# Optimization experiments

Hardware: AMD Instinct MI355X
Metric: run time of the kernel (lower is better)

Reference implementation:

```python
import jax, jax.numpy as jnp
import numpy as np

K = 2        # capsules
ROUTIT = 3   # routing iterations
DD = 32      # per-capsule dim
D = K * DD   # 64
NEG = -1e9
EPS_NORM = 1e-12


def _l2norm_caps(c, n):
    # F.normalize over last dim of [n, K, DD]
    c = c.reshape(n, K, DD)
    nrm = jnp.sqrt((c * c).sum(axis=2, keepdims=True))
    c = c / jnp.maximum(nrm, EPS_NORM)
    return c.reshape(n, D)


def disen_encoder(x, W, b, src_trg):
    n = x.shape[0]
    src, trg = src_trg[0], src_trg[1]
    x = x @ W + b                               # [n, D]
    x = _l2norm_caps(x, n)
    z = x[src].reshape(-1, K, DD)               # [m, K, DD] per-edge source capsules
    c = x
    for _ in range(ROUTIT):
        ct = c[trg].reshape(-1, K, DD)          # gather target capsules
        p = jax.nn.softmax((z * ct).sum(axis=2), axis=1)   # [m, K]
        ws = (p[:, :, None] * z).reshape(-1, D)            # [m, D]
        c = c.at[trg].add(ws)                   # scatter-aggregate (index_add_)
        c = _l2norm_caps(c, n)
    return c


def attention_fuse(z, W1, b1, W2):
    # z: [n, 3, D]
    w = jax.nn.leaky_relu(z @ W1 + b1, negative_slope=0.2) @ W2   # [n, 3, 1]
    beta = jax.nn.softmax(w, axis=1) + 1e-6
    beta = beta / beta.sum(axis=1, keepdims=True)
    return (beta * z).sum(axis=1)               # [n, D]


def masked_softmax(vec, mask):
    m = mask.astype(vec.dtype)
    return jax.nn.softmax(vec * m + (1.0 - m) * NEG, axis=-1)


def joint_update(user, item, A, Wj, bj):
    tu = jax.nn.relu(user @ Wj + bj)
    ti = jax.nn.relu(item @ Wj + bj)
    ui = user @ item.T                          # [N, M]
    uw = masked_softmax(ui, A > 0)
    upd_user = tu + uw @ item
    iw = masked_softmax(ui.T, A.T > 0)
    upd_item = ti + iw @ user
    return upd_user, upd_item


def setup_inputs() -> dict:
    key = jax.random.key(0)
    ks = jax.random.split(key, 24)
    N_NC, N_D, E_NC, E_D = 10240, 5120, 327680, 163840
    inp = {
        'NC_1': jax.random.normal(ks[0], (N_NC, 599), jnp.float32),
        'NC_2': jax.random.normal(ks[1], (N_NC, 599), jnp.float32),
        'NC_3': jax.random.normal(ks[2], (N_NC, 599), jnp.float32),
        'D_1': jax.random.normal(ks[3], (N_D, 91), jnp.float32),
        'D_2': jax.random.normal(ks[4], (N_D, 91), jnp.float32),
        'D_3': jax.random.normal(ks[5], (N_D, 91), jnp.float32),
        'edge_indexNC1': jax.random.randint(ks[6], (2, E_NC), 0, N_NC, jnp.int32),
        'edge_indexNC2': jax.random.randint(ks[7], (2, E_NC), 0, N_NC, jnp.int32),
        'edge_indexNC3': jax.random.randint(ks[8], (2, E_NC), 0, N_NC, jnp.int32),
        'edge_indexD1': jax.random.randint(ks[9], (2, E_D), 0, N_D, jnp.int32),
        'edge_indexD2': jax.random.randint(ks[10], (2, E_D), 0, N_D, jnp.int32),
        'edge_indexD3': jax.random.randint(ks[11], (2, E_D), 0, N_D, jnp.int32),
        'heterogeneous': jnp.zeros((1,), jnp.float32),
        'heterogeneous1': jnp.zeros((1,), jnp.float32),
        'A': jax.random.randint(ks[12], (N_NC, N_D), 0, 2, jnp.int32).astype(jnp.float32),
        'L': jnp.zeros((1,), jnp.float32),
    }
    def xavier(k, shape):
        lim = float(np.sqrt(6.0 / (shape[0] + shape[1])))
        return jax.random.uniform(k, shape, jnp.float32, -lim, lim)
    inp['W_nc'] = xavier(ks[13], (599, D)); inp['b_nc'] = jnp.zeros((D,), jnp.float32)
    inp['W_d'] = xavier(ks[14], (91, D));   inp['b_d'] = jnp.zeros((D,), jnp.float32)
    inp['attn_W1'] = xavier(ks[15], (D, D)); inp['attn_b1'] = jnp.zeros((D,), jnp.float32)
    inp['attn_W2'] = xavier(ks[16], (D, 1))
    inp['joint_W'] = xavier(ks[17], (D, D)); inp['joint_b'] = jnp.zeros((D,), jnp.float32)
    return inp


def reference(NC_1, NC_2, NC_3, D_1, D_2, D_3,
              edge_indexNC1, edge_indexNC2, edge_indexNC3,
              edge_indexD1, edge_indexD2, edge_indexD3,
              heterogeneous, heterogeneous1, A, L,
              W_nc, b_nc, W_d, b_d, attn_W1, attn_b1, attn_W2, joint_W, joint_b):
    nc1 = disen_encoder(NC_1, W_nc, b_nc, edge_indexNC1)
    d1 = disen_encoder(D_1, W_d, b_d, edge_indexD1)
    nc2 = disen_encoder(NC_2, W_nc, b_nc, edge_indexNC2)
    d2 = disen_encoder(D_2, W_d, b_d, edge_indexD2)
    nc3 = disen_encoder(NC_3, W_nc, b_nc, edge_indexNC3)
    d3 = disen_encoder(D_3, W_d, b_d, edge_indexD3)
    nc = attention_fuse(jnp.stack([nc1, nc2, nc3], axis=1), attn_W1, attn_b1, attn_W2)
    d = attention_fuse(jnp.stack([d1, d2, d3], axis=1), attn_W1, attn_b1, attn_W2)
    nc, d = joint_update(nc, d, A, joint_W, joint_b)
    return d @ nc.T   # decoder1 with identity act: [N_d, N_nc]
```

## Files before the change

kernel.cpp:

```cpp
#include <hip/hip_runtime.h>
#include <hip/hip_bf16.h>
#include <stdint.h>

using bf16x8 = __attribute__((ext_vector_type(8))) short;
using f32x4  = __attribute__((ext_vector_type(4))) float;

__device__ __forceinline__ unsigned short f2b(float f) {
  unsigned u = __float_as_uint(f);
  u = u + 0x7FFFu + ((u >> 16) & 1u);
  return (unsigned short)(u >> 16);
}
__device__ __forceinline__ float b2f(unsigned short s) {
  return __uint_as_float(((unsigned)s) << 16);
}

#define N_NC 10240
#define N_D  5120
#define E_NC 327680
#define E_D  163840
#define F_NC 599
#define F_D  91
#define KP_NC 608
#define KP_D  96
#define TOT_NODES 46080
#define TOT_EDGES 1474560
#define MW 160

__global__ __launch_bounds__(256) void k_zero(int* p, int n) {
  int t = blockIdx.x * 256 + threadIdx.x;
  if (t < n) p[t] = 0;
}

__global__ __launch_bounds__(256) void k_prep(const float* Wnc, const float* Wd,
                       unsigned short* WTnc_hi, unsigned short* WTnc_lo,
                       unsigned short* WTd_hi, unsigned short* WTd_lo) {
  int tid = blockIdx.x * blockDim.x + threadIdx.x;
  int stride = gridDim.x * blockDim.x;
  for (int i = tid; i < 64 * KP_NC; i += stride) {
    int d = i / KP_NC, k = i % KP_NC;
    float w = (k < F_NC) ? Wnc[k * 64 + d] : 0.0f;
    unsigned short h = f2b(w);
    WTnc_hi[i] = h;
    WTnc_lo[i] = f2b(w - b2f(h));
  }
  for (int i = tid; i < 64 * KP_D; i += stride) {
    int d = i / KP_D, k = i % KP_D;
    float w = (k < F_D) ? Wd[k * 64 + d] : 0.0f;
    unsigned short h = f2b(w);
    WTd_hi[i] = h;
    WTd_lo[i] = f2b(w - b2f(h));
  }
}

template <int F, int KPAD>
__global__ __launch_bounds__(256) void k_encoder(const float* __restrict__ x,
    const unsigned short* __restrict__ WT_hi, const unsigned short* __restrict__ WT_lo,
    const float* __restrict__ bias, float* __restrict__ out) {
  int wave = threadIdx.x >> 6;
  int tile = blockIdx.x * 4 + wave;
  int l = threadIdx.x & 63;
  int h = l >> 4, r0 = l & 15;
  int m0 = tile * 16;

  f32x4 acc[4] = {{0,0,0,0},{0,0,0,0},{0,0,0,0},{0,0,0,0}};
  const float* xrow = x + (size_t)(m0 + r0) * F;

  for (int ks = 0; ks < KPAD / 32; ++ks) {
    int k0 = ks * 32 + h * 8;
    bf16x8 ah, al;
#pragma unroll
    for (int j = 0; j < 8; ++j) {
      int k = k0 + j;
      float v = (k < F) ? xrow[k] : 0.0f;
      unsigned short hb = f2b(v);
      ah[j] = (short)hb;
      al[j] = (short)f2b(v - b2f(hb));
    }
#pragma unroll
    for (int nt = 0; nt < 4; ++nt) {
      bf16x8 bh = *(const bf16x8*)(WT_hi + (nt * 16 + r0) * KPAD + k0);
      bf16x8 bl = *(const bf16x8*)(WT_lo + (nt * 16 + r0) * KPAD + k0);
      acc[nt] = __builtin_amdgcn_mfma_f32_16x16x32_bf16(ah, bh, acc[nt], 0, 0, 0);
      acc[nt] = __builtin_amdgcn_mfma_f32_16x16x32_bf16(ah, bl, acc[nt], 0, 0, 0);
      acc[nt] = __builtin_amdgcn_mfma_f32_16x16x32_bf16(al, bh, acc[nt], 0, 0, 0);
    }
  }
#pragma unroll
  for (int nt = 0; nt < 4; ++nt) {
    float bv = bias[nt * 16 + r0];
#pragma unroll
    for (int r = 0; r < 4; ++r) acc[nt][r] += bv;
  }
#pragma unroll
  for (int r = 0; r < 4; ++r) {
    float ss0 = acc[0][r] * acc[0][r] + acc[1][r] * acc[1][r];
    float ss1 = acc[2][r] * acc[2][r] + acc[3][r] * acc[3][r];
#pragma unroll
    for (int m = 1; m < 16; m <<= 1) { ss0 += __shfl_xor(ss0, m); ss1 += __shfl_xor(ss1, m); }
    float s0 = 1.0f / fmaxf(sqrtf(ss0), 1e-12f);
    float s1 = 1.0f / fmaxf(sqrtf(ss1), 1e-12f);
    float* o = out + (size_t)(m0 + 4 * h + r) * 64;
    o[ 0 + r0] = acc[0][r] * s0;
    o[16 + r0] = acc[1][r] * s0;
    o[32 + r0] = acc[2][r] * s1;
    o[48 + r0] = acc[3][r] * s1;
  }
}

__device__ __forceinline__ void seg_decode(int t,
    const int* e0, const int* e1, const int* e2,
    const int* e3, const int* e4, const int* e5,
    const int** ep, int* el, int* noff, int* En) {
  if (t < 3 * E_NC) {
    int g = t / E_NC; *el = t - g * E_NC; *En = E_NC; *noff = g * N_NC;
    *ep = (g == 0) ? e0 : (g == 1) ? e1 : e2;
  } else {
    int u = t - 3 * E_NC;
    int g = u / E_D; *el = u - g * E_D; *En = E_D; *noff = 3 * N_NC + g * N_D;
    *ep = (g == 0) ? e3 : (g == 1) ? e4 : e5;
  }
}

__global__ __launch_bounds__(256) void k_hist(const int* e0, const int* e1, const int* e2,
                       const int* e3, const int* e4, const int* e5, int* cnt) {
  int t = blockIdx.x * blockDim.x + threadIdx.x;
  const int* ep; int el, noff, En;
  seg_decode(t, e0, e1, e2, e3, e4, e5, &ep, &el, &noff, &En);
  int trg = ep[En + el];
  atomicAdd(&cnt[noff + trg], 1);
}

__global__ __launch_bounds__(256) void k_scan1(const int* cnt, int* incl, int* bsum) {
  __shared__ int sh[256];
  int g = blockIdx.x * 256 + threadIdx.x;
  int v = cnt[g];
  sh[threadIdx.x] = v;
  __syncthreads();
  for (int off = 1; off < 256; off <<= 1) {
    int t = (threadIdx.x >= off) ? sh[threadIdx.x - off] : 0;
    __syncthreads();
    sh[threadIdx.x] += t;
    __syncthreads();
  }
  incl[g] = sh[threadIdx.x];
  if (threadIdx.x == 255) bsum[blockIdx.x] = sh[255];
}

__global__ __launch_bounds__(256) void k_scan2(int* bsum) {
  __shared__ int sh[256];
  int t = threadIdx.x;
  int v = (t < 180) ? bsum[t] : 0;
  sh[t] = v;
  __syncthreads();
  for (int off = 1; off < 256; off <<= 1) {
    int x = (t >= off) ? sh[t - off] : 0;
    __syncthreads();
    sh[t] += x;
    __syncthreads();
  }
  if (t < 180) bsum[t] = sh[t] - v;
}

__global__ __launch_bounds__(256) void k_scan3(const int* incl, const int* cnt,
                                               const int* bsum, int* rowptr, int* cursor) {
  int g = blockIdx.x * 256 + threadIdx.x;
  int x = incl[g] + bsum[blockIdx.x];
  rowptr[g + 1] = x;
  cursor[g] = x - cnt[g];
  if (g == 0) rowptr[0] = 0;
}

__global__ __launch_bounds__(256) void k_scatter(const int* e0, const int* e1, const int* e2,
                          const int* e3, const int* e4, const int* e5,
                          int* cursor, int* csr) {
  int t = blockIdx.x * blockDim.x + threadIdx.x;
  const int* ep; int el, noff, En;
  seg_decode(t, e0, e1, e2, e3, e4, e5, &ep, &el, &noff, &En);
  int src = ep[el];
  int trg = ep[En + el];
  int pos = atomicAdd(&cursor[noff + trg], 1);
  csr[pos] = src;
}

template <int NPG>
__global__ __launch_bounds__(256) void k_route(const float* __restrict__ xnorm, float* __restrict__ cfin,
    const int* __restrict__ row_ptr, const int* __restrict__ csr, int rpOff) {
  int node = (blockIdx.x * blockDim.x + threadIdx.x) >> 5;
  int q = threadIdx.x & 31;
  int graph = node / NPG;
  size_t gb32 = (size_t)graph * NPG * 32;
  int rp0 = row_ptr[rpOff + node], rp1 = row_ptr[rpOff + node + 1];
  const float2* xn2 = (const float2*)xnorm;
  float2 c = xn2[(size_t)node * 32 + q];
  for (int it = 0; it < 3; ++it) {
    float2 acc = c;
    for (int e = rp0; e < rp1; ++e) {
      int s = csr[e];
      float2 z = xn2[gb32 + (size_t)s * 32 + q];
      float part = z.x * c.x + z.y * c.y;
      part += __shfl_xor(part, 1);
      part += __shfl_xor(part, 2);
      part += __shfl_xor(part, 4);
      part += __shfl_xor(part, 8);
      float other = __shfl_xor(part, 16);
      float p = 1.0f / (1.0f + __expf(other - part));
      acc.x += p * z.x;
      acc.y += p * z.y;
    }
    float ss = acc.x * acc.x + acc.y * acc.y;
    ss += __shfl_xor(ss, 1);
    ss += __shfl_xor(ss, 2);
    ss += __shfl_xor(ss, 4);
    ss += __shfl_xor(ss, 8);
    float sc = 1.0f / fmaxf(sqrtf(ss), 1e-12f);
    c.x = acc.x * sc;
    c.y = acc.y * sc;
  }
  ((float2*)cfin)[(size_t)node * 32 + q] = c;
}

__global__ __launch_bounds__(256) void k_attn(const float* __restrict__ cfin, int n,
    const float* __restrict__ W1, const float* __restrict__ b1, const float* __restrict__ W2,
    const float* __restrict__ Wj, const float* __restrict__ bj,
    unsigned short* bfr, unsigned short* bfT, float* tu) {
  __shared__ float zs[4][3][64];
  __shared__ float fs[4][64];
  int wave = threadIdx.x >> 6, l = threadIdx.x & 63;
  int node = blockIdx.x * 4 + wave;
#pragma unroll
  for (int j = 0; j < 3; ++j)
    zs[wave][j][l] = cfin[((size_t)j * n + node) * 64 + l];
  __syncthreads();
  float w[3];
#pragma unroll
  for (int j = 0; j < 3; ++j) {
    float y = b1[l];
    for (int k = 0; k < 64; ++k) y += zs[wave][j][k] * W1[k * 64 + l];
    y = (y > 0.0f) ? y : 0.2f * y;
    float t = y * W2[l];
#pragma unroll
    for (int m = 1; m < 64; m <<= 1) t += __shfl_xor(t, m);
    w[j] = t;
  }
  float mx = fmaxf(w[0], fmaxf(w[1], w[2]));
  float e0 = __expf(w[0] - mx), e1 = __expf(w[1] - mx), e2 = __expf(w[2] - mx);
  float inv = 1.0f / (e0 + e1 + e2);
  float be0 = e0 * inv + 1e-6f, be1 = e1 * inv + 1e-6f, be2 = e2 * inv + 1e-6f;
  float bs = 1.0f / (be0 + be1 + be2);
  be0 *= bs; be1 *= bs; be2 *= bs;
  float o = be0 * zs[wave][0][l] + be1 * zs[wave][1][l] + be2 * zs[wave][2][l];
  fs[wave][l] = o;
  __syncthreads();
  bfr[(size_t)node * 64 + l] = f2b(o);
  bfT[(size_t)l * n + node] = f2b(o);
  float t = bj[l];
  for (int k = 0; k < 64; ++k) t += fs[wave][k] * Wj[k * 64 + l];
  tu[(size_t)node * 64 + l] = fmaxf(t, 0.0f);
}

__global__ __launch_bounds__(256) void k_mask(const float* __restrict__ A, unsigned int* mb) {
  int wid = (blockIdx.x * blockDim.x + threadIdx.x) >> 6;
  int l = threadIdx.x & 63;
  int row = wid / 10, seg = wid % 10;
  const float4* ap = (const float4*)(A + (size_t)row * 5120 + seg * 512 + l * 8);
  float4 v0 = ap[0], v1 = ap[1];
  unsigned b = (unsigned)(v0.x > 0.0f)       | ((unsigned)(v0.y > 0.0f) << 1)
             | ((unsigned)(v0.z > 0.0f) << 2) | ((unsigned)(v0.w > 0.0f) << 3)
             | ((unsigned)(v1.x > 0.0f) << 4) | ((unsigned)(v1.y > 0.0f) << 5)
             | ((unsigned)(v1.z > 0.0f) << 6) | ((unsigned)(v1.w > 0.0f) << 7);
  b |= ((unsigned)__shfl_xor((int)b, 1)) << 8;
  b |= ((unsigned)__shfl_xor((int)b, 2)) << 16;
  if ((l & 3) == 0) mb[row * MW + seg * 16 + (l >> 2)] = b;
}

template <bool MT>
__global__ __launch_bounds__(256) void k_joint(const unsigned short* __restrict__ qbf,
    const unsigned short* __restrict__ kbf, const unsigned short* __restrict__ vT, int Nk,
    const unsigned int* __restrict__ mb, const float* __restrict__ tu,
    unsigned short* outh, unsigned short* outl) {
  __shared__ float st[4][16][2];
  __shared__ __align__(16) unsigned short pl[4][16][32];
  __shared__ float oc[4][16][64];
  int wave = threadIdx.x >> 6, l = threadIdx.x & 63;
  int h = l >> 4, r0 = l & 15;
  int q0 = blockIdx.x * 16;
  int seg = Nk >> 2;
  int m_lo = wave * seg, m_hi = m_lo + seg;

  bf16x8 a0 = *(const bf16x8*)(qbf + (size_t)(q0 + r0) * 64 + h * 8);
  bf16x8 a1 = *(const bf16x8*)(qbf + (size_t)(q0 + r0) * 64 + 32 + h * 8);

  float lm[4], ls[4];
#pragma unroll
  for (int r = 0; r < 4; ++r) { lm[r] = -1e30f; ls[r] = 0.0f; }

  for (int m0 = m_lo; m0 < m_hi; m0 += 32) {
    f32x4 s0 = {0,0,0,0}, s1 = {0,0,0,0};
    {
      bf16x8 b00 = *(const bf16x8*)(kbf + (size_t)(m0 + r0) * 64 + h * 8);
      bf16x8 b10 = *(const bf16x8*)(kbf + (size_t)(m0 + 16 + r0) * 64 + h * 8);
      s0 = __builtin_amdgcn_mfma_f32_16x16x32_bf16(a0, b00, s0, 0, 0, 0);
      s1 = __builtin_amdgcn_mfma_f32_16x16x32_bf16(a0, b10, s1, 0, 0, 0);
      bf16x8 b01 = *(const bf16x8*)(kbf + (size_t)(m0 + r0) * 64 + 32 + h * 8);
      bf16x8 b11 = *(const bf16x8*)(kbf + (size_t)(m0 + 16 + r0) * 64 + 32 + h * 8);
      s0 = __builtin_amdgcn_mfma_f32_16x16x32_bf16(a1, b01, s0, 0, 0, 0);
      s1 = __builtin_amdgcn_mfma_f32_16x16x32_bf16(a1, b11, s1, 0, 0, 0);
    }
    unsigned w0 = 0, w1 = 0;
    if (MT) {
      w0 = mb[(size_t)(m0 + r0) * MW + (q0 >> 5)];
      w1 = mb[(size_t)(m0 + 16 + r0) * MW + (q0 >> 5)];
    }
#pragma unroll
    for (int r = 0; r < 4; ++r) {
      float e0, e1;
      if (MT) {
        int bit = (q0 & 31) + 4 * h + r;
        e0 = ((w0 >> bit) & 1u) ? s0[r] : -1e9f;
        e1 = ((w1 >> bit) & 1u) ? s1[r] : -1e9f;
      } else {
        unsigned wr = mb[(size_t)(q0 + 4 * h + r) * MW + (m0 >> 5)];
        e0 = ((wr >> r0) & 1u) ? s0[r] : -1e9f;
        e1 = ((wr >> (r0 + 16)) & 1u) ? s1[r] : -1e9f;
      }
      float nm = fmaxf(lm[r], fmaxf(e0, e1));
      ls[r] = ls[r] * __expf(lm[r] - nm) + __expf(e0 - nm) + __expf(e1 - nm);
      lm[r] = nm;
    }
  }
#pragma unroll
  for (int r = 0; r < 4; ++r) {
#pragma unroll
    for (int m = 1; m < 16; m <<= 1) {
      float om = __shfl_xor(lm[r], m), os = __shfl_xor(ls[r], m);
      float nm = fmaxf(lm[r], om);
      ls[r] = ls[r] * __expf(lm[r] - nm) + os * __expf(om - nm);
      lm[r] = nm;
    }
  }
  if (r0 == 0) {
#pragma unroll
    for (int r = 0; r < 4; ++r) { st[wave][4 * h + r][0] = lm[r]; st[wave][4 * h + r][1] = ls[r]; }
  }
  __syncthreads();
  float M[4], S[4];
#pragma unroll
  for (int r = 0; r < 4; ++r) {
    int row = 4 * h + r;
    float mm = fmaxf(fmaxf(st[0][row][0], st[1][row][0]), fmaxf(st[2][row][0], st[3][row][0]));
    float s = st[0][row][1] * __expf(st[0][row][0] - mm)
            + st[1][row][1] * __expf(st[1][row][0] - mm)
            + st[2][row][1] * __expf(st[2][row][0] - mm)
            + st[3][row][1] * __expf(st[3][row][0] - mm);
    M[r] = mm; S[r] = s;
  }

  f32x4 o[4] = {{0,0,0,0},{0,0,0,0},{0,0,0,0},{0,0,0,0}};
  for (int m0 = m_lo; m0 < m_hi; m0 += 32) {
    f32x4 s0 = {0,0,0,0}, s1 = {0,0,0,0};
    {
      bf16x8 b00 = *(const bf16x8*)(kbf + (size_t)(m0 + r0) * 64 + h * 8);
      bf16x8 b10 = *(const bf16x8*)(kbf + (size_t)(m0 + 16 + r0) * 64 + h * 8);
      s0 = __builtin_amdgcn_mfma_f32_16x16x32_bf16(a0, b00, s0, 0, 0, 0);
      s1 = __builtin_amdgcn_mfma_f32_16x16x32_bf16(a0, b10, s1, 0, 0, 0);
      bf16x8 b01 = *(const bf16x8*)(kbf + (size_t)(m0 + r0) * 64 + 32 + h * 8);
      bf16x8 b11 = *(const bf16x8*)(kbf + (size_t)(m0 + 16 + r0) * 64 + 32 + h * 8);
      s0 = __builtin_amdgcn_mfma_f32_16x16x32_bf16(a1, b01, s0, 0, 0, 0);
      s1 = __builtin_amdgcn_mfma_f32_16x16x32_bf16(a1, b11, s1, 0, 0, 0);
    }
    unsigned w0 = 0, w1 = 0;
    if (MT) {
      w0 = mb[(size_t)(m0 + r0) * MW + (q0 >> 5)];
      w1 = mb[(size_t)(m0 + 16 + r0) * MW + (q0 >> 5)];
    }
#pragma unroll
    for (int r = 0; r < 4; ++r) {
      float e0, e1;
      if (MT) {
        int bit = (q0 & 31) + 4 * h + r;
        e0 = ((w0 >> bit) & 1u) ? s0[r] : -1e9f;
        e1 = ((w1 >> bit) & 1u) ? s1[r] : -1e9f;
      } else {
        unsigned wr = mb[(size_t)(q0 + 4 * h + r) * MW + (m0 >> 5)];
        e0 = ((wr >> r0) & 1u) ? s0[r] : -1e9f;
        e1 = ((wr >> (r0 + 16)) & 1u) ? s1[r] : -1e9f;
      }
      pl[wave][4 * h + r][r0]      = f2b(__expf(e0 - M[r]));
      pl[wave][4 * h + r][r0 + 16] = f2b(__expf(e1 - M[r]));
    }
    __syncthreads();
    bf16x8 pa = *(const bf16x8*)(&pl[wave][r0][h * 8]);
#pragma unroll
    for (int nt = 0; nt < 4; ++nt) {
      bf16x8 bv = *(const bf16x8*)(vT + (size_t)(nt * 16 + r0) * Nk + m0 + h * 8);
      o[nt] = __builtin_amdgcn_mfma_f32_16x16x32_bf16(pa, bv, o[nt], 0, 0, 0);
    }
  }
  float inv[4];
#pragma unroll
  for (int r = 0; r < 4; ++r) inv[r] = 1.0f / S[r];
#pragma unroll
  for (int nt = 0; nt < 4; ++nt)
#pragma unroll
    for (int r = 0; r < 4; ++r)
      oc[wave][4 * h + r][nt * 16 + r0] = o[nt][r] * inv[r];
  __syncthreads();
  for (int e = threadIdx.x; e < 1024; e += 256) {
    int row = e >> 6, col = e & 63;
    float v = oc[0][row][col] + oc[1][row][col] + oc[2][row][col] + oc[3][row][col];
    v += tu[(size_t)(q0 + row) * 64 + col];
    unsigned short hb = f2b(v);
    outh[(size_t)(q0 + row) * 64 + col] = hb;
    outl[(size_t)(q0 + row) * 64 + col] = f2b(v - b2f(hb));
  }
}

__global__ __launch_bounds__(256) void k_dec(const unsigned short* __restrict__ Ih,
    const unsigned short* __restrict__ Il,
    const unsigned short* __restrict__ Uh, const unsigned short* __restrict__ Ul,
    float* __restrict__ out) {
  int w = (blockIdx.x * blockDim.x + threadIdx.x) >> 6;
  int l = threadIdx.x & 63, h = l >> 4, r0 = l & 15;
  int i0 = (w / 160) * 16, u0 = (w % 160) * 64;
  size_t abase = (size_t)(i0 + r0) * 64 + h * 8;
  bf16x8 a0h = *(const bf16x8*)(Ih + abase);
  bf16x8 a1h = *(const bf16x8*)(Ih + abase + 32);
  bf16x8 a0l = *(const bf16x8*)(Il + abase);
  bf16x8 a1l = *(const bf16x8*)(Il + abase + 32);
#pragma unroll
  for (int nt = 0; nt < 4; ++nt) {
    size_t bbase = (size_t)(u0 + nt * 16 + r0) * 64 + h * 8;
    bf16x8 b0h = *(const bf16x8*)(Uh + bbase);
    bf16x8 b1h = *(const bf16x8*)(Uh + bbase + 32);
    bf16x8 b0l = *(const bf16x8*)(Ul + bbase);
    bf16x8 b1l = *(const bf16x8*)(Ul + bbase + 32);
    f32x4 acc = {0,0,0,0};
    acc = __builtin_amdgcn_mfma_f32_16x16x32_bf16(a0h, b0h, acc, 0, 0, 0);
    acc = __builtin_amdgcn_mfma_f32_16x16x32_bf16(a1h, b1h, acc, 0, 0, 0);
    acc = __builtin_amdgcn_mfma_f32_16x16x32_bf16(a0h, b0l, acc, 0, 0, 0);
    acc = __builtin_amdgcn_mfma_f32_16x16x32_bf16(a1h, b1l, acc, 0, 0, 0);
    acc = __builtin_amdgcn_mfma_f32_16x16x32_bf16(a0l, b0h, acc, 0, 0, 0);
    acc = __builtin_amdgcn_mfma_f32_16x16x32_bf16(a1l, b1h, acc, 0, 0, 0);
#pragma unroll
    for (int r = 0; r < 4; ++r)
      out[(size_t)(i0 + 4 * h + r) * 10240 + u0 + nt * 16 + r0] = acc[r];
  }
}

extern "C" void kernel_launch(void* const* d_in, const int* in_sizes, int n_in,
                              void* d_out, int out_size, void* d_ws, size_t ws_size,
                              hipStream_t stream) {
  const float* NC1 = (const float*)d_in[0];
  const float* NC2 = (const float*)d_in[1];
  const float* NC3 = (const float*)d_in[2];
  const float* Dx1 = (const float*)d_in[3];
  const float* Dx2 = (const float*)d_in[4];
  const float* Dx3 = (const float*)d_in[5];
  const int* e0 = (const int*)d_in[6];
  const int* e1 = (const int*)d_in[7];
  const int* e2 = (const int*)d_in[8];
  const int* e3 = (const int*)d_in[9];
  const int* e4 = (const int*)d_in[10];
  const int* e5 = (const int*)d_in[11];
  const float* A   = (const float*)d_in[14];
  const float* Wnc = (const float*)d_in[16];
  const float* bnc = (const float*)d_in[17];
  const float* Wd  = (const float*)d_in[18];
  const float* bd  = (const float*)d_in[19];
  const float* W1  = (const float*)d_in[20];
  const float* b1  = (const float*)d_in[21];
  const float* W2  = (const float*)d_in[22];
  const float* Wj  = (const float*)d_in[23];
  const float* bj  = (const float*)d_in[24];
  (void)in_sizes; (void)n_in; (void)out_size; (void)ws_size;

  char* ob = (char*)d_out;
  char* ws = (char*)d_ws;

  float* xn_nc = (float*)(ob);
  float* xn_d  = (float*)(ob + 7864320);
  float* cf_nc = (float*)(ob + 11796480);
  float* cf_d  = (float*)(ob + 19660800);
  int* cnt    = (int*)(ob + 23592960);
  int* incl   = (int*)(ob + 23592960 + 184320);
  int* bsum   = (int*)(ob + 23592960 + 368640);
  int* rowptr = (int*)(ob + 23592960 + 369664);
  int* cursor = (int*)(ob + 23592960 + 554240);
  int* csr    = (int*)(ob + 23592960 + 738560);
  unsigned int* mb = (unsigned int*)(ob + 23592960);
  unsigned short* ubf  = (unsigned short*)(ob);
  unsigned short* ubfT = (unsigned short*)(ob + 1310720);
  unsigned short* ibf  = (unsigned short*)(ob + 2621440);
  unsigned short* ibfT = (unsigned short*)(ob + 3276800);
  float* tu            = (float*)(ob + 3932160);
  float* ti            = (float*)(ob + 6553600);

  unsigned short* udUh = (unsigned short*)(ws);
  unsigned short* udUl = (unsigned short*)(ws + 1310720);
  unsigned short* udIh = (unsigned short*)(ws + 2621440);
  unsigned short* udIl = (unsigned short*)(ws + 3276800);
  unsigned short* WTnc_hi = (unsigned short*)(ws + 3932160);
  unsigned short* WTnc_lo = (unsigned short*)(ws + 4009984);
  unsigned short* WTd_hi  = (unsigned short*)(ws + 4087808);
  unsigned short* WTd_lo  = (unsigned short*)(ws + 4100096);

  k_prep<<<64, 256, 0, stream>>>(Wnc, Wd, WTnc_hi, WTnc_lo, WTd_hi, WTd_lo);

  k_encoder<F_NC, KP_NC><<<160, 256, 0, stream>>>(NC1, WTnc_hi, WTnc_lo, bnc, xn_nc);
  k_encoder<F_NC, KP_NC><<<160, 256, 0, stream>>>(NC2, WTnc_hi, WTnc_lo, bnc, xn_nc + (size_t)N_NC * 64);
  k_encoder<F_NC, KP_NC><<<160, 256, 0, stream>>>(NC3, WTnc_hi, WTnc_lo, bnc, xn_nc + (size_t)2 * N_NC * 64);
  k_encoder<F_D, KP_D><<<80, 256, 0, stream>>>(Dx1, WTd_hi, WTd_lo, bd, xn_d);
  k_encoder<F_D, KP_D><<<80, 256, 0, stream>>>(Dx2, WTd_hi, WTd_lo, bd, xn_d + (size_t)N_D * 64);
  k_encoder<F_D, KP_D><<<80, 256, 0, stream>>>(Dx3, WTd_hi, WTd_lo, bd, xn_d + (size_t)2 * N_D * 64);

  k_zero<<<180, 256, 0, stream>>>(cnt, TOT_NODES);
  k_hist<<<TOT_EDGES / 256, 256, 0, stream>>>(e0, e1, e2, e3, e4, e5, cnt);
  k_scan1<<<180, 256, 0, stream>>>(cnt, incl, bsum);
  k_scan2<<<1, 256, 0, stream>>>(bsum);
  k_scan3<<<180, 256, 0, stream>>>(incl, cnt, bsum, rowptr, cursor);
  k_scatter<<<TOT_EDGES / 256, 256, 0, stream>>>(e0, e1, e2, e3, e4, e5, cursor, csr);

  k_route<N_NC><<<(3 * N_NC) / 8, 256, 0, stream>>>(xn_nc, cf_nc, rowptr, csr, 0);
  k_route<N_D><<<(3 * N_D) / 8, 256, 0, stream>>>(xn_d, cf_d, rowptr, csr, 3 * N_NC);

  k_mask<<<25600, 256, 0, stream>>>(A, mb);

  k_attn<<<N_NC / 4, 256, 0, stream>>>(cf_nc, N_NC, W1, b1, W2, Wj, bj, ubf, ubfT, tu);
  k_attn<<<N_D / 4, 256, 0, stream>>>(cf_d, N_D, W1, b1, W2, Wj, bj, ibf, ibfT, ti);

  k_joint<false><<<N_NC / 16, 256, 0, stream>>>(ubf, ibf, ibfT, N_D, mb, tu, udUh, udUl);
  k_joint<true><<<N_D / 16, 256, 0, stream>>>(ibf, ubf, ubfT, N_NC, mb, ti, udIh, udIl);

  k_dec<<<(N_D / 16) * (N_NC / 64) / 4, 256, 0, stream>>>(udIh, udIl, udUh, udUl, (float*)d_out);
}
```

Baseline: 1.618 ms.

## Fuse masked softmax into a single pass without max subtraction

Replaces the two-pass masked softmax in the joint-attention kernel with one pass. The first pass computed the running max and sum; the second recomputed QK^T and built P·V. Because the user and item embeddings are built from L2-normalised capsules, their dot products are bounded, so exp is applied to raw scores and normalisation is deferred to the final reduction. This halves the score MFMAs and the K loads, drops the per-iteration barrier (the P tile is private to each wave), and pads the P tile in shared memory. The trade-off is that a row with no unmasked entries now outputs zeros rather than the reference's uniform distribution.

```diff
diff --git a/kernel.cpp b/kernel.cpp
--- a/kernel.cpp
+++ b/kernel.cpp
@@ -278,9 +278,9 @@
     const unsigned short* __restrict__ kbf, const unsigned short* __restrict__ vT, int Nk,
     const unsigned int* __restrict__ mb, const float* __restrict__ tu,
     unsigned short* outh, unsigned short* outl) {
-  __shared__ float st[4][16][2];
-  __shared__ __align__(16) unsigned short pl[4][16][32];
+  __shared__ __align__(16) unsigned short pl[4][16][40];
   __shared__ float oc[4][16][64];
+  __shared__ float ssum[4][16];
   int wave = threadIdx.x >> 6, l = threadIdx.x & 63;
   int h = l >> 4, r0 = l & 15;
   int q0 = blockIdx.x * 16;
@@ -290,22 +290,21 @@
   bf16x8 a0 = *(const bf16x8*)(qbf + (size_t)(q0 + r0) * 64 + h * 8);
   bf16x8 a1 = *(const bf16x8*)(qbf + (size_t)(q0 + r0) * 64 + 32 + h * 8);
 
-  float lm[4], ls[4];
-#pragma unroll
-  for (int r = 0; r < 4; ++r) { lm[r] = -1e30f; ls[r] = 0.0f; }
-
+  f32x4 o[4] = {{0,0,0,0},{0,0,0,0},{0,0,0,0},{0,0,0,0}};
+  float ls[4] = {0.0f, 0.0f, 0.0f, 0.0f};
+
+#pragma unroll 2
   for (int m0 = m_lo; m0 < m_hi; m0 += 32) {
     f32x4 s0 = {0,0,0,0}, s1 = {0,0,0,0};
-    {
-      bf16x8 b00 = *(const bf16x8*)(kbf + (size_t)(m0 + r0) * 64 + h * 8);
-      bf16x8 b10 = *(const bf16x8*)(kbf + (size_t)(m0 + 16 + r0) * 64 + h * 8);
-      s0 = __builtin_amdgcn_mfma_f32_16x16x32_bf16(a0, b00, s0, 0, 0, 0);
-      s1 = __builtin_amdgcn_mfma_f32_16x16x32_bf16(a0, b10, s1, 0, 0, 0);
-      bf16x8 b01 = *(const bf16x8*)(kbf + (size_t)(m0 + r0) * 64 + 32 + h * 8);
-      bf16x8 b11 = *(const bf16x8*)(kbf + (size_t)(m0 + 16 + r0) * 64 + 32 + h * 8);
-      s0 = __builtin_amdgcn_mfma_f32_16x16x32_bf16(a1, b01, s0, 0, 0, 0);
-      s1 = __builtin_amdgcn_mfma_f32_16x16x32_bf16(a1, b11, s1, 0, 0, 0);
-    }
+    bf16x8 b00 = *(const bf16x8*)(kbf + (size_t)(m0 + r0) * 64 + h * 8);
+    bf16x8 b10 = *(const bf16x8*)(kbf + (size_t)(m0 + 16 + r0) * 64 + h * 8);
+    bf16x8 b01 = *(const bf16x8*)(kbf + (size_t)(m0 + r0) * 64 + 32 + h * 8);
+    bf16x8 b11 = *(const bf16x8*)(kbf + (size_t)(m0 + 16 + r0) * 64 + 32 + h * 8);
+    s0 = __builtin_amdgcn_mfma_f32_16x16x32_bf16(a0, b00, s0, 0, 0, 0);
+    s1 = __builtin_amdgcn_mfma_f32_16x16x32_bf16(a0, b10, s1, 0, 0, 0);
+    s0 = __builtin_amdgcn_mfma_f32_16x16x32_bf16(a1, b01, s0, 0, 0, 0);
+    s1 = __builtin_amdgcn_mfma_f32_16x16x32_bf16(a1, b11, s1, 0, 0, 0);
+
     unsigned w0 = 0, w1 = 0;
     if (MT) {
       w0 = mb[(size_t)(m0 + r0) * MW + (q0 >> 5)];
@@ -313,82 +312,20 @@
     }
 #pragma unroll
     for (int r = 0; r < 4; ++r) {
-      float e0, e1;
+      float p0, p1;
       if (MT) {
         int bit = (q0 & 31) + 4 * h + r;
-        e0 = ((w0 >> bit) & 1u) ? s0[r] : -1e9f;
-        e1 = ((w1 >> bit) & 1u) ? s1[r] : -1e9f;
+        p0 = ((w0 >> bit) & 1u) ? __expf(s0[r]) : 0.0f;
+        p1 = ((w1 >> bit) & 1u) ? __expf(s1[r]) : 0.0f;
       } else {
         unsigned wr = mb[(size_t)(q0 + 4 * h + r) * MW + (m0 >> 5)];
-        e0 = ((wr >> r0) & 1u) ? s0[r] : -1e9f;
-        e1 = ((wr >> (r0 + 16)) & 1u) ? s1[r] : -1e9f;
+        p0 = ((wr >> r0) & 1u) ? __expf(s0[r]) : 0.0f;
+        p1 = ((wr >> (r0 + 16)) & 1u) ? __expf(s1[r]) : 0.0f;
       }
-      float nm = fmaxf(lm[r], fmaxf(e0, e1));
-      ls[r] = ls[r] * __expf(lm[r] - nm) + __expf(e0 - nm) + __expf(e1 - nm);
-      lm[r] = nm;
-    }
-  }
-#pragma unroll
-  for (int r = 0; r < 4; ++r) {
-#pragma unroll
-    for (int m = 1; m < 16; m <<= 1) {
-      float om = __shfl_xor(lm[r], m), os = __shfl_xor(ls[r], m);
-      float nm = fmaxf(lm[r], om);
-      ls[r] = ls[r] * __expf(lm[r] - nm) + os * __expf(om - nm);
-      lm[r] = nm;
-    }
-  }
-  if (r0 == 0) {
-#pragma unroll
-    for (int r = 0; r < 4; ++r) { st[wave][4 * h + r][0] = lm[r]; st[wave][4 * h + r][1] = ls[r]; }
-  }
-  __syncthreads();
-  float M[4], S[4];
-#pragma unroll
-  for (int r = 0; r < 4; ++r) {
-    int row = 4 * h + r;
-    float mm = fmaxf(fmaxf(st[0][row][0], st[1][row][0]), fmaxf(st[2][row][0], st[3][row][0]));
-    float s = st[0][row][1] * __expf(st[0][row][0] - mm)
-            + st[1][row][1] * __expf(st[1][row][0] - mm)
-            + st[2][row][1] * __expf(st[2][row][0] - mm)
-            + st[3][row][1] * __expf(st[3][row][0] - mm);
-    M[r] = mm; S[r] = s;
-  }
-
-  f32x4 o[4] = {{0,0,0,0},{0,0,0,0},{0,0,0,0},{0,0,0,0}};
-  for (int m0 = m_lo; m0 < m_hi; m0 += 32) {
-    f32x4 s0 = {0,0,0,0}, s1 = {0,0,0,0};
-    {
-      bf16x8 b00 = *(const bf16x8*)(kbf + (size_t)(m0 + r0) * 64 + h * 8);
-      bf16x8 b10 = *(const bf16x8*)(kbf + (size_t)(m0 + 16 + r0) * 64 + h * 8);
-      s0 = __builtin_amdgcn_mfma_f32_16x16x32_bf16(a0, b00, s0, 0, 0, 0);
-      s1 = __builtin_amdgcn_mfma_f32_16x16x32_bf16(a0, b10, s1, 0, 0, 0);
-      bf16x8 b01 = *(const bf16x8*)(kbf + (size_t)(m0 + r0) * 64 + 32 + h * 8);
-      bf16x8 b11 = *(const bf16x8*)(kbf + (size_t)(m0 + 16 + r0) * 64 + 32 + h * 8);
-      s0 = __builtin_amdgcn_mfma_f32_16x16x32_bf16(a1, b01, s0, 0, 0, 0);
-      s1 = __builtin_amdgcn_mfma_f32_16x16x32_bf16(a1, b11, s1, 0, 0, 0);
-    }
-    unsigned w0 = 0, w1 = 0;
-    if (MT) {
-      w0 = mb[(size_t)(m0 + r0) * MW + (q0 >> 5)];
-      w1 = mb[(size_t)(m0 + 16 + r0) * MW + (q0 >> 5)];
-    }
-#pragma unroll
-    for (int r = 0; r < 4; ++r) {
-      float e0, e1;
-      if (MT) {
-        int bit = (q0 & 31) + 4 * h + r;
-        e0 = ((w0 >> bit) & 1u) ? s0[r] : -1e9f;
-        e1 = ((w1 >> bit) & 1u) ? s1[r] : -1e9f;
-      } else {
-        unsigned wr = mb[(size_t)(q0 + 4 * h + r) * MW + (m0 >> 5)];
-        e0 = ((wr >> r0) & 1u) ? s0[r] : -1e9f;
-        e1 = ((wr >> (r0 + 16)) & 1u) ? s1[r] : -1e9f;
-      }
-      pl[wave][4 * h + r][r0]      = f2b(__expf(e0 - M[r]));
-      pl[wave][4 * h + r][r0 + 16] = f2b(__expf(e1 - M[r]));
-    }
-    __syncthreads();
+      ls[r] += p0 + p1;
+      pl[wave][4 * h + r][r0]      = f2b(p0);
+      pl[wave][4 * h + r][r0 + 16] = f2b(p1);
+    }
     bf16x8 pa = *(const bf16x8*)(&pl[wave][r0][h * 8]);
 #pragma unroll
     for (int nt = 0; nt < 4; ++nt) {
@@ -396,19 +333,27 @@
       o[nt] = __builtin_amdgcn_mfma_f32_16x16x32_bf16(pa, bv, o[nt], 0, 0, 0);
     }
   }
-  float inv[4];
-#pragma unroll
-  for (int r = 0; r < 4; ++r) inv[r] = 1.0f / S[r];
+
+#pragma unroll
+  for (int r = 0; r < 4; ++r) {
+#pragma unroll
+    for (int m = 1; m < 16; m <<= 1) ls[r] += __shfl_xor(ls[r], m);
+  }
+  if (r0 == 0) {
+#pragma unroll
+    for (int r = 0; r < 4; ++r) ssum[wave][4 * h + r] = ls[r];
+  }
 #pragma unroll
   for (int nt = 0; nt < 4; ++nt)
 #pragma unroll
     for (int r = 0; r < 4; ++r)
-      oc[wave][4 * h + r][nt * 16 + r0] = o[nt][r] * inv[r];
+      oc[wave][4 * h + r][nt * 16 + r0] = o[nt][r];
   __syncthreads();
   for (int e = threadIdx.x; e < 1024; e += 256) {
     int row = e >> 6, col = e & 63;
     float v = oc[0][row][col] + oc[1][row][col] + oc[2][row][col] + oc[3][row][col];
-    v += tu[(size_t)(q0 + row) * 64 + col];
+    float S = ssum[0][row] + ssum[1][row] + ssum[2][row] + ssum[3][row];
+    v = v / fmaxf(S, 1e-30f) + tu[(size_t)(q0 + row) * 64 + col];
     unsigned short hb = f2b(v);
     outh[(size_t)(q0 + row) * 64 + col] = hb;
     outl[(size_t)(q0 + row) * 64 + col] = f2b(v - b2f(hb));
```

Result: faster. 1.428 ms (-11.8%).
